# Kernel tuning notes

Measured on AMD Instinct MI355X. Metric: run time of the kernel, lower is better.

The kernel has to match this reference:

```python
import jax, jax.numpy as jnp
import numpy as np

D_MODEL = 1024
NUM_HEADS = 16
D_K = D_MODEL // NUM_HEADS  # 64


def setup_inputs() -> dict:
    key = jax.random.key(0)
    k1, k2, k3, k4, k5 = jax.random.split(key, 5)
    scale = 1.0 / np.sqrt(D_MODEL)
    x = jax.random.normal(k1, (2, 8192, D_MODEL), dtype=jnp.float32)
    W_qkv = jax.random.normal(k2, (D_MODEL, 3 * D_MODEL), dtype=jnp.float32) * scale
    b_qkv = jax.random.normal(k3, (3 * D_MODEL,), dtype=jnp.float32) * 0.01
    W_out = jax.random.normal(k4, (D_MODEL, D_MODEL), dtype=jnp.float32) * scale
    b_out = jax.random.normal(k5, (D_MODEL,), dtype=jnp.float32) * 0.01
    return {"x": x, "W_qkv": W_qkv, "b_qkv": b_qkv, "W_out": W_out, "b_out": b_out}


def reference(x, W_qkv, b_qkv, W_out, b_out):
    B, S, _ = x.shape
    # qkv: [B, S, 3*d_model] -> reshape [B, S, H, 3*d_k] (matches torch reshape:
    # head h owns contiguous slice [h*3dk:(h+1)*3dk], split into q/k/v of d_k each)
    qkv = (jnp.einsum('bsd,de->bse', x, W_qkv) + b_qkv).reshape(B, S, NUM_HEADS, 3 * D_K)
    q, k, v = qkv[..., :D_K], qkv[..., D_K:2 * D_K], qkv[..., 2 * D_K:]
    # NOTE: faithful to source — no head transpose, so matmul contracts d_k and
    # produces scores across the HEAD axis: [B, S, H, H]
    scores = jnp.einsum('bshd,bsgd->bshg', q, k) / np.sqrt(D_K)
    attn = jax.nn.softmax(scores, axis=-1)  # softmax over heads (g)
    context = jnp.einsum('bshg,bsgd->bshd', attn, v).reshape(B, S, NUM_HEADS * D_K)
    return jnp.einsum('bsd,de->bse', context, W_out) + b_out
```

## Files before the change

### kernel.cpp

```cpp
#include <hip/hip_runtime.h>
#include <hip/hip_bf16.h>

typedef short bf16x8 __attribute__((ext_vector_type(8)));
typedef float f32x4 __attribute__((ext_vector_type(4)));
typedef ushort ushort8_t __attribute__((ext_vector_type(8)));

__device__ __forceinline__ float bf2f(ushort u) {
    union { unsigned int i; float f; } c; c.i = ((unsigned int)u) << 16; return c.f;
}
__device__ __forceinline__ ushort f2bf(float f) {
    union { float f; unsigned int i; } c; c.f = f;
    unsigned int x = c.i;
    return (ushort)((x + 0x7fffu + ((x >> 16) & 1u)) >> 16);
}

#define GLOAD_LDS16(g, l) __builtin_amdgcn_global_load_lds( \
    (const __attribute__((address_space(1))) unsigned int*)(g), \
    (__attribute__((address_space(3))) unsigned int*)(l), 16, 0, 0)

__global__ __launch_bounds__(256) void k_cvt_bf16(const float* __restrict__ in,
                                                  ushort* __restrict__ out, int n4) {
    int i = blockIdx.x * 256 + threadIdx.x;
    if (i < n4) {
        float4 v = ((const float4*)in)[i];
        ushort4 o;
        o.x = f2bf(v.x); o.y = f2bf(v.y); o.z = f2bf(v.z); o.w = f2bf(v.w);
        ((ushort4*)out)[i] = o;
    }
}

__global__ __launch_bounds__(256) void k_transpose_cvt(const float* __restrict__ in,
                                                       ushort* __restrict__ out,
                                                       int K, int N) {
    __shared__ float tile[32][33];
    int n0 = blockIdx.x * 32, k0 = blockIdx.y * 32;
    int tx = threadIdx.x, ty = threadIdx.y;
    #pragma unroll
    for (int i = 0; i < 32; i += 8)
        tile[ty + i][tx] = in[(size_t)(k0 + ty + i) * N + n0 + tx];
    __syncthreads();
    #pragma unroll
    for (int i = 0; i < 32; i += 8)
        out[(size_t)(n0 + ty + i) * K + k0 + tx] = f2bf(tile[tx][ty + i]);
}


#define LDSA(c,kk) (lds + (c)*65536 + (kk)*16384)
#define LDSB(c,kk) (lds + (c)*65536 + 32768 + (kk)*16384)
#define STAGE_A(c,kk,col) do { \
    GLOAD_LDS16(gA0 + (col), LDSA(c,kk) + wave*1024); \
    GLOAD_LDS16(gA1 + (col), LDSA(c,kk) + 8192 + wave*1024); } while(0)
#define STAGE_B(c,kk,col) do { \
    GLOAD_LDS16(gB0 + (col), LDSB(c,kk) + wave*1024); \
    GLOAD_LDS16(gB1 + (col), LDSB(c,kk) + 8192 + wave*1024); } while(0)
#define READ_A8(c,kk) do { const char* _p = LDSA(c,kk) + aoff; \
    _Pragma("unroll") for (int m = 0; m < 8; ++m) af[m] = *(const bf16x8*)(_p + m*1024); } while(0)
#define READ_B2(c,kk,n0) do { const char* _p = LDSB(c,kk) + boff; \
    bfr[n0] = *(const bf16x8*)(_p + (n0)*1024); \
    bfr[(n0)+1] = *(const bf16x8*)(_p + ((n0)+1)*1024); } while(0)
#define MF16(n0) do { __builtin_amdgcn_s_setprio(1); \
    _Pragma("unroll") for (int m = 0; m < 8; ++m) { \
    acc[m][n0]     = __builtin_amdgcn_mfma_f32_16x16x32_bf16(af[m], bfr[n0],     acc[m][n0],     0,0,0); \
    acc[m][(n0)+1] = __builtin_amdgcn_mfma_f32_16x16x32_bf16(af[m], bfr[(n0)+1], acc[m][(n0)+1], 0,0,0); } \
    __builtin_amdgcn_s_setprio(0); } while(0)

#define BAR __builtin_amdgcn_s_barrier()
#define SB0 __builtin_amdgcn_sched_barrier(0)
#define VM10 asm volatile("s_waitcnt vmcnt(10)")
#define VM0  asm volatile("s_waitcnt vmcnt(0)")

#define PH1(reads, stage, mf, vm) do { reads; stage; mf; SB0; vm; BAR; SB0; } while(0)

#define ITERX(kb, LAST) do { \
   PH1( { READ_A8(0,0); READ_B2(0,0,0); }, STAGE_B(1,1,(kb)+96),              MF16(0), ); \
   PH1( { READ_B2(0,0,2); },               if(!(LAST)) STAGE_A(0,0,(kb)+128), MF16(2), if(LAST) VM0; else VM10 ); \
   PH1( { READ_A8(0,1); READ_B2(0,1,0); }, if(!(LAST)) STAGE_B(0,0,(kb)+128), MF16(0), ); \
   PH1( { READ_B2(0,1,2); },               if(!(LAST)) STAGE_A(0,1,(kb)+160), MF16(2), if(!(LAST)) VM10 ); \
   PH1( { READ_A8(1,0); READ_B2(1,0,0); }, if(!(LAST)) STAGE_B(0,1,(kb)+160), MF16(0), ); \
   PH1( { READ_B2(1,0,2); },               if(!(LAST)) STAGE_A(1,0,(kb)+192), MF16(2), if(!(LAST)) VM10 ); \
   PH1( { READ_A8(1,1); READ_B2(1,1,0); }, if(!(LAST)) STAGE_B(1,0,(kb)+192), MF16(0), ); \
   PH1( { READ_B2(1,1,2); },               if(!(LAST)) STAGE_A(1,1,(kb)+224), MF16(2), if(!(LAST)) VM10 ); \
} while(0)

template<bool OUT_BF16>
__global__ __launch_bounds__(512, 2) void k_gemm256(const ushort* __restrict__ A,
                                                    const ushort* __restrict__ Bt,
                                                    const float* __restrict__ bias,
                                                    void* __restrict__ Cout,
                                                    int N, int NTN) {
    __shared__ __align__(16) char lds[131072];
    const int K = 1024;
    const int tid = threadIdx.x;
    const int wave = tid >> 6, lane = tid & 63;
    const int wr = wave >> 2, wc = wave & 3;
    const int r = lane & 15, q = lane >> 4;

    const int cpx = gridDim.x >> 3, wg = blockIdx.x;
    const int swz = (wg & 7) * cpx + (wg >> 3);
    const int tm = swz / NTN, tn = swz - tm * NTN;
    const int bm = tm * 256, bn = tn * 256;

    const int srow = tid >> 2;
    const int c16l = (tid & 3) ^ ((srow >> 1) & 3);
    const ushort* gA0 = A  + (size_t)(bm + srow) * K + c16l * 8;
    const ushort* gA1 = gA0 + (size_t)128 * K;
    const ushort* gB0 = Bt + (size_t)(bn + srow) * K + c16l * 8;
    const ushort* gB1 = gB0 + (size_t)128 * K;

    const int chunkx = ((q ^ ((r >> 1) & 3)) << 4);
    const int aoff = (wr * 128 + r) * 64 + chunkx;
    const int boff = (wc * 64 + r) * 64 + chunkx;

    f32x4 acc[8][4];
    #pragma unroll
    for (int m = 0; m < 8; ++m)
        #pragma unroll
        for (int n = 0; n < 4; ++n)
            acc[m][n] = (f32x4){0.f, 0.f, 0.f, 0.f};
    bf16x8 af[8], bfr[4];

    STAGE_A(0,0,0);  STAGE_B(0,0,0);
    STAGE_A(0,1,32); STAGE_B(0,1,32);
    STAGE_A(1,0,64); STAGE_B(1,0,64);
    STAGE_A(1,1,96);
    VM10; BAR; SB0;

    #pragma unroll 1
    for (int i = 0; i < 7; ++i) { ITERX(i * 128, 0); }
    ITERX(896, 1);

    float* Cf = (float*)Cout;
    ushort* Cb = (ushort*)Cout;
    #pragma unroll
    for (int m = 0; m < 8; ++m) {
        int row0 = bm + wr * 128 + m * 16 + q * 4;
        #pragma unroll
        for (int n = 0; n < 4; ++n) {
            int col = bn + wc * 64 + n * 16 + r;
            float bv = bias[col];
            #pragma unroll
            for (int j = 0; j < 4; ++j) {
                float v = acc[m][n][j] + bv;
                if (OUT_BF16) Cb[(size_t)(row0 + j) * N + col] = f2bf(v);
                else          Cf[(size_t)(row0 + j) * N + col] = v;
            }
        }
    }
}

__global__ __launch_bounds__(256) void k_attn_mfma(const ushort* __restrict__ qkv,
                                                   ushort* __restrict__ ctx) {
    const int lane = threadIdx.x & 63;
    const size_t tok = (size_t)blockIdx.x * 4 + (threadIdx.x >> 6);
    const ushort* row = qkv + tok * 3072;
    const int r = lane & 15, g = lane >> 4;

    bf16x8 ka[2], qb[2];
    #pragma unroll
    for (int c = 0; c < 2; ++c) {
        ka[c] = *(const bf16x8*)(row + r * 192 + 64 + c * 32 + g * 8);
        qb[c] = *(const bf16x8*)(row + r * 192 +      c * 32 + g * 8);
    }
    f32x4 st = (f32x4){0.f, 0.f, 0.f, 0.f};
    st = __builtin_amdgcn_mfma_f32_16x16x32_bf16(ka[0], qb[0], st, 0, 0, 0);
    st = __builtin_amdgcn_mfma_f32_16x16x32_bf16(ka[1], qb[1], st, 0, 0, 0);

    float s[4];
    #pragma unroll
    for (int j = 0; j < 4; ++j) s[j] = st[j] * 0.125f;
    float m = fmaxf(fmaxf(s[0], s[1]), fmaxf(s[2], s[3]));
    m = fmaxf(m, __shfl_xor(m, 16));
    m = fmaxf(m, __shfl_xor(m, 32));
    float p[4], sum = 0.f;
    #pragma unroll
    for (int j = 0; j < 4; ++j) { p[j] = __expf(s[j] - m); sum += p[j]; }
    sum += __shfl_xor(sum, 16);
    sum += __shfl_xor(sum, 32);
    float inv = 1.f / sum;
    #pragma unroll
    for (int j = 0; j < 4; ++j) p[j] *= inv;

    const bool gok = (g < 2);
    const int src0 = (r + 32 * g) & 63, src1 = (src0 + 16) & 63;
    bf16x8 pa;
    #pragma unroll
    for (int j = 0; j < 4; ++j) {
        float a0 = __shfl(p[j], src0, 64);
        float a1 = __shfl(p[j], src1, 64);
        pa[j]     = (short)(gok ? f2bf(a0) : (ushort)0);
        pa[4 + j] = (short)(gok ? f2bf(a1) : (ushort)0);
    }

    #pragma unroll
    for (int db = 0; db < 4; ++db) {
        bf16x8 vb;
        #pragma unroll
        for (int j = 0; j < 8; ++j)
            vb[j] = (short)(gok ? row[(g * 8 + j) * 192 + 128 + db * 16 + r] : (ushort)0);
        f32x4 o = (f32x4){0.f, 0.f, 0.f, 0.f};
        o = __builtin_amdgcn_mfma_f32_16x16x32_bf16(pa, vb, o, 0, 0, 0);
        #pragma unroll
        for (int j = 0; j < 4; ++j)
            ctx[tok * 1024 + (4 * g + j) * 64 + db * 16 + r] = f2bf(o[j]);
    }
}

extern "C" void kernel_launch(void* const* d_in, const int* in_sizes, int n_in,
                              void* d_out, int out_size, void* d_ws, size_t ws_size,
                              hipStream_t stream) {
    const float* x     = (const float*)d_in[0];
    const float* W_qkv = (const float*)d_in[1];
    const float* b_qkv = (const float*)d_in[2];
    const float* W_out = (const float*)d_in[3];
    const float* b_out = (const float*)d_in[4];

    const int M = 16384, D = 1024, N3 = 3072;

    ushort* xb   = (ushort*)d_ws;
    ushort* wqkT = xb + (size_t)M * D;
    ushort* woT  = wqkT + (size_t)N3 * D;
    ushort* qkv  = woT + (size_t)D * D;
    ushort* ctx  = xb;

    hipLaunchKernelGGL(k_cvt_bf16, dim3((M * D / 4 + 255) / 256), dim3(256), 0, stream,
                       x, xb, M * D / 4);
    hipLaunchKernelGGL(k_transpose_cvt, dim3(N3 / 32, D / 32), dim3(32, 8), 0, stream,
                       W_qkv, wqkT, D, N3);
    hipLaunchKernelGGL(k_transpose_cvt, dim3(D / 32, D / 32), dim3(32, 8), 0, stream,
                       W_out, woT, D, D);
    hipLaunchKernelGGL((k_gemm256<true>), dim3((N3 / 256) * (M / 256)), dim3(512), 0, stream,
                       xb, wqkT, b_qkv, (void*)qkv, N3, N3 / 256);
    hipLaunchKernelGGL(k_attn_mfma, dim3(M / 4), dim3(256), 0, stream, qkv, ctx);
    hipLaunchKernelGGL((k_gemm256<false>), dim3((D / 256) * (M / 256)), dim3(512), 0, stream,
                       ctx, woT, b_out, d_out, D, D / 256);
}
```

Measured before the change: 201.4 us.

## Switch GEMM to 32x32x16 MFMA with restructured four-phase pipeline

Replaces the 16x16x32 bf16 MFMA tiling in the 256x256 GEMM with 32x32x16 MFMA tiles (4x2 f32x16 accumulators per wave). The LDS read pattern and swizzle offsets are rewritten for 32-row fragments, and the K loop is regrouped from eight half-phases into four phases that each read A and B once and issue all MFMAs, with staging and vmcnt waits rebalanced. The goal is fewer LDS reads per FLOP and fewer barriers per K step. In exchange, each phase issues a larger burst of loads and the epilogue store pattern changes.

After: 209.3 us. +3.9%, slower.

```diff
diff --git a/kernel.cpp b/kernel.cpp
--- a/kernel.cpp
+++ b/kernel.cpp
@@ -3,6 +3,7 @@
 
 typedef short bf16x8 __attribute__((ext_vector_type(8)));
 typedef float f32x4 __attribute__((ext_vector_type(4)));
+typedef float f32x16 __attribute__((ext_vector_type(16)));
 typedef ushort ushort8_t __attribute__((ext_vector_type(8)));
 
 __device__ __forceinline__ float bf2f(ushort u) {
@@ -53,33 +54,39 @@
 #define STAGE_B(c,kk,col) do { \
     GLOAD_LDS16(gB0 + (col), LDSB(c,kk) + wave*1024); \
     GLOAD_LDS16(gB1 + (col), LDSB(c,kk) + 8192 + wave*1024); } while(0)
-#define READ_A8(c,kk) do { const char* _p = LDSA(c,kk) + aoff; \
-    _Pragma("unroll") for (int m = 0; m < 8; ++m) af[m] = *(const bf16x8*)(_p + m*1024); } while(0)
-#define READ_B2(c,kk,n0) do { const char* _p = LDSB(c,kk) + boff; \
-    bfr[n0] = *(const bf16x8*)(_p + (n0)*1024); \
-    bfr[(n0)+1] = *(const bf16x8*)(_p + ((n0)+1)*1024); } while(0)
-#define MF16(n0) do { __builtin_amdgcn_s_setprio(1); \
-    _Pragma("unroll") for (int m = 0; m < 8; ++m) { \
-    acc[m][n0]     = __builtin_amdgcn_mfma_f32_16x16x32_bf16(af[m], bfr[n0],     acc[m][n0],     0,0,0); \
-    acc[m][(n0)+1] = __builtin_amdgcn_mfma_f32_16x16x32_bf16(af[m], bfr[(n0)+1], acc[m][(n0)+1], 0,0,0); } \
+
+#define READ_R(c,kk32) do { \
+    const char* _pa = LDSA(c,kk32) + arow; const char* _pb = LDSB(c,kk32) + brow; \
+    _Pragma("unroll") for (int mt = 0; mt < 4; ++mt) { \
+        af[mt*2+0] = *(const bf16x8*)(_pa + mt*2048 + swz0); \
+        af[mt*2+1] = *(const bf16x8*)(_pa + mt*2048 + swz1); } \
+    _Pragma("unroll") for (int nt = 0; nt < 2; ++nt) { \
+        bfv[nt*2+0] = *(const bf16x8*)(_pb + nt*2048 + swz0); \
+        bfv[nt*2+1] = *(const bf16x8*)(_pb + nt*2048 + swz1); } } while(0)
+
+#define MF32ALL() do { __builtin_amdgcn_s_setprio(1); \
+    _Pragma("unroll") for (int mt = 0; mt < 4; ++mt) \
+    _Pragma("unroll") for (int nt = 0; nt < 2; ++nt) { \
+        f32x16 a = acc[mt][nt]; \
+        a = __builtin_amdgcn_mfma_f32_32x32x16_bf16(af[mt*2+0], bfv[nt*2+0], a, 0,0,0); \
+        a = __builtin_amdgcn_mfma_f32_32x32x16_bf16(af[mt*2+1], bfv[nt*2+1], a, 0,0,0); \
+        acc[mt][nt] = a; } \
     __builtin_amdgcn_s_setprio(0); } while(0)
 
 #define BAR __builtin_amdgcn_s_barrier()
 #define SB0 __builtin_amdgcn_sched_barrier(0)
 #define VM10 asm volatile("s_waitcnt vmcnt(10)")
+#define VM8  asm volatile("s_waitcnt vmcnt(8)")
+#define VM4  asm volatile("s_waitcnt vmcnt(4)")
 #define VM0  asm volatile("s_waitcnt vmcnt(0)")
 
-#define PH1(reads, stage, mf, vm) do { reads; stage; mf; SB0; vm; BAR; SB0; } while(0)
-
-#define ITERX(kb, LAST) do { \
-   PH1( { READ_A8(0,0); READ_B2(0,0,0); }, STAGE_B(1,1,(kb)+96),              MF16(0), ); \
-   PH1( { READ_B2(0,0,2); },               if(!(LAST)) STAGE_A(0,0,(kb)+128), MF16(2), if(LAST) VM0; else VM10 ); \
-   PH1( { READ_A8(0,1); READ_B2(0,1,0); }, if(!(LAST)) STAGE_B(0,0,(kb)+128), MF16(0), ); \
-   PH1( { READ_B2(0,1,2); },               if(!(LAST)) STAGE_A(0,1,(kb)+160), MF16(2), if(!(LAST)) VM10 ); \
-   PH1( { READ_A8(1,0); READ_B2(1,0,0); }, if(!(LAST)) STAGE_B(0,1,(kb)+160), MF16(0), ); \
-   PH1( { READ_B2(1,0,2); },               if(!(LAST)) STAGE_A(1,0,(kb)+192), MF16(2), if(!(LAST)) VM10 ); \
-   PH1( { READ_A8(1,1); READ_B2(1,1,0); }, if(!(LAST)) STAGE_B(1,0,(kb)+192), MF16(0), ); \
-   PH1( { READ_B2(1,1,2); },               if(!(LAST)) STAGE_A(1,1,(kb)+224), MF16(2), if(!(LAST)) VM10 ); \
+#define PH32(c,kk32, stage, vm) do { READ_R(c,kk32); stage; MF32ALL(); SB0; vm; BAR; SB0; } while(0)
+
+#define ITER32(kb, LAST) do { \
+  PH32(0,0, STAGE_B(1,1,(kb)+96), VM8); \
+  PH32(0,1, if(!(LAST)){ STAGE_A(0,0,(kb)+128); STAGE_B(0,0,(kb)+128); }, if(LAST) VM4; else VM8); \
+  PH32(1,0, if(!(LAST)){ STAGE_A(0,1,(kb)+160); STAGE_B(0,1,(kb)+160); }, if(LAST) VM0; else VM8); \
+  PH32(1,1, if(!(LAST)){ STAGE_A(1,0,(kb)+192); STAGE_B(1,0,(kb)+192); STAGE_A(1,1,(kb)+224); }, if(!(LAST)) VM10); \
 } while(0)
 
 template<bool OUT_BF16>
@@ -93,7 +100,7 @@
     const int tid = threadIdx.x;
     const int wave = tid >> 6, lane = tid & 63;
     const int wr = wave >> 2, wc = wave & 3;
-    const int r = lane & 15, q = lane >> 4;
+    const int r32 = lane & 31, lh = lane >> 5;
 
     const int cpx = gridDim.x >> 3, wg = blockIdx.x;
     const int swz = (wg & 7) * cpx + (wg >> 3);
@@ -107,45 +114,48 @@
     const ushort* gB0 = Bt + (size_t)(bn + srow) * K + c16l * 8;
     const ushort* gB1 = gB0 + (size_t)128 * K;
 
-    const int chunkx = ((q ^ ((r >> 1) & 3)) << 4);
-    const int aoff = (wr * 128 + r) * 64 + chunkx;
-    const int boff = (wc * 64 + r) * 64 + chunkx;
-
-    f32x4 acc[8][4];
-    #pragma unroll
-    for (int m = 0; m < 8; ++m)
-        #pragma unroll
-        for (int n = 0; n < 4; ++n)
-            acc[m][n] = (f32x4){0.f, 0.f, 0.f, 0.f};
-    bf16x8 af[8], bfr[4];
-
-    STAGE_A(0,0,0);  STAGE_B(0,0,0);
-    STAGE_A(0,1,32); STAGE_B(0,1,32);
-    STAGE_A(1,0,64); STAGE_B(1,0,64);
+    const int sw3 = (r32 >> 1) & 3;
+    const int arow = (wr * 128 + r32) * 64;
+    const int brow = (wc * 64 + r32) * 64;
+    const int swz0 = ((0 * 2 + lh) ^ sw3) << 4;
+    const int swz1 = ((1 * 2 + lh) ^ sw3) << 4;
+
+    f32x16 acc[4][2];
+    #pragma unroll
+    for (int mt = 0; mt < 4; ++mt)
+        #pragma unroll
+        for (int nt = 0; nt < 2; ++nt)
+            #pragma unroll
+            for (int j = 0; j < 16; ++j)
+                acc[mt][nt][j] = 0.f;
+    bf16x8 af[8], bfv[4];
+
+    STAGE_B(0,0,0);  STAGE_A(0,0,0);
+    STAGE_B(0,1,32); STAGE_A(0,1,32);
+    STAGE_B(1,0,64); STAGE_A(1,0,64);
     STAGE_A(1,1,96);
     VM10; BAR; SB0;
 
     #pragma unroll 1
-    for (int i = 0; i < 7; ++i) { ITERX(i * 128, 0); }
-    ITERX(896, 1);
+    for (int i = 0; i < 7; ++i) { ITER32(i * 128, 0); }
+    ITER32(896, 1);
 
     float* Cf = (float*)Cout;
     ushort* Cb = (ushort*)Cout;
     #pragma unroll
-    for (int m = 0; m < 8; ++m) {
-        int row0 = bm + wr * 128 + m * 16 + q * 4;
-        #pragma unroll
-        for (int n = 0; n < 4; ++n) {
-            int col = bn + wc * 64 + n * 16 + r;
+    for (int mt = 0; mt < 4; ++mt)
+        #pragma unroll
+        for (int nt = 0; nt < 2; ++nt) {
+            int col = bn + wc * 64 + nt * 32 + r32;
             float bv = bias[col];
             #pragma unroll
-            for (int j = 0; j < 4; ++j) {
-                float v = acc[m][n][j] + bv;
-                if (OUT_BF16) Cb[(size_t)(row0 + j) * N + col] = f2bf(v);
-                else          Cf[(size_t)(row0 + j) * N + col] = v;
+            for (int j = 0; j < 16; ++j) {
+                int row = bm + wr * 128 + mt * 32 + (j & 3) + 8 * (j >> 2) + 4 * lh;
+                float v = acc[mt][nt][j] + bv;
+                if (OUT_BF16) Cb[(size_t)row * N + col] = f2bf(v);
+                else          Cf[(size_t)row * N + col] = v;
             }
         }
-    }
 }
 
 __global__ __launch_bounds__(256) void k_attn_mfma(const ushort* __restrict__ qkv,
```
